# Optimization experiments

Hardware: AMD Instinct MI355X
Metric: run time of the kernel (lower is better)

The kernel has to match this reference:

```python
import jax, jax.numpy as jnp
import numpy as np

EPS = 1e-6  # eps assumed for rms/unit norm (repo uses a small eps; math identical up to eps)

def rms_norm(x):
    # normalize so RMS over last dim == 1
    return x * jax.lax.rsqrt(jnp.mean(x * x, axis=-1, keepdims=True) + EPS)

def unit_norm(w):
    # normalize each output row of the weight to unit L2 norm
    return w * jax.lax.rsqrt(jnp.sum(w * w, axis=-1, keepdims=True) + EPS)

def setup_inputs() -> dict:
    key = jax.random.key(0)
    k1, k2, k3 = jax.random.split(key, 3)
    B, S, D = 4, 2048, 2048
    x = jax.random.normal(k1, (B, S, D), dtype=jnp.float32)
    w_in = jax.random.normal(k2, (3 * D, D), dtype=jnp.float32)
    w_out = jax.random.normal(k3, (D, D), dtype=jnp.float32)
    return {"x": x, "w_in": w_in, "w_out": w_out}

def reference(x, w_in, w_out):
    B, S, D = x.shape
    H = 16
    hd = D // H
    # MPLinear in-projection with unit-normalized weight rows
    qkv = jnp.einsum("bsd,fd->bsf", x, unit_norm(w_in))  # [B,S,3D]
    qkv = qkv.reshape(B, S, 3, H, hd).transpose(2, 0, 3, 1, 4)  # [3,B,H,S,hd]
    q, k, v = qkv[0], qkv[1], qkv[2]
    q = rms_norm(q)
    k = rms_norm(k)
    # scaled dot product attention, causal, default scale 1/sqrt(hd)
    scores = jnp.einsum("bhqd,bhkd->bhqk", q, k) / jnp.sqrt(jnp.float32(hd))
    causal_mask = jnp.tril(jnp.ones((S, S), dtype=bool))
    scores = jnp.where(causal_mask, scores, jnp.finfo(scores.dtype).min)
    attn = jax.nn.softmax(scores, axis=-1)
    a = jnp.einsum("bhqk,bhkd->bhqd", attn, v)  # [B,H,S,hd]
    a = rms_norm(a)
    a = a.transpose(0, 2, 1, 3).reshape(B, S, D)
    return jnp.einsum("bsd,fd->bsf", a, unit_norm(w_out))
```

## Files before the change

### kernel.cpp

```cpp
#include <hip/hip_runtime.h>

typedef float f32x4 __attribute__((ext_vector_type(4)));
typedef __bf16 bf16x8 __attribute__((ext_vector_type(8)));

#define EPSF 1e-6f
#define AS1 __attribute__((address_space(1)))
#define AS3 __attribute__((address_space(3)))

__device__ static inline void gl_lds16(const __bf16* g, __bf16* l) {
  __builtin_amdgcn_global_load_lds((const AS1 void*)g, (AS3 void*)l, 16, 0, 0);
}

__global__ __launch_bounds__(256) void prep(const float* __restrict__ x,
                                            const float* __restrict__ w_in,
                                            const float* __restrict__ w_out,
                                            __bf16* __restrict__ xb,
                                            __bf16* __restrict__ w_in_n,
                                            __bf16* __restrict__ w_out_n) {
  __shared__ float red[4];
  const int bid = blockIdx.x;
  const int t = threadIdx.x;
  if (bid < 8192) {
    const float* src = (bid < 6144) ? (w_in + (size_t)bid * 2048)
                                    : (w_out + (size_t)(bid - 6144) * 2048);
    __bf16* dst = (bid < 6144) ? (w_in_n + (size_t)bid * 2048)
                               : (w_out_n + (size_t)(bid - 6144) * 2048);
    float4 v[2];
    float ss = 0.f;
#pragma unroll
    for (int i = 0; i < 2; i++) {
      v[i] = ((const float4*)src)[t + i * 256];
      ss += v[i].x * v[i].x + v[i].y * v[i].y + v[i].z * v[i].z + v[i].w * v[i].w;
    }
#pragma unroll
    for (int m = 32; m >= 1; m >>= 1) ss += __shfl_xor(ss, m);
    if ((t & 63) == 0) red[t >> 6] = ss;
    __syncthreads();
    float tot = red[0] + red[1] + red[2] + red[3];
    float sc = rsqrtf(tot + EPSF);
#pragma unroll
    for (int i = 0; i < 2; i++) {
      int c0 = (t + i * 256) * 4;
      dst[c0 + 0] = (__bf16)(v[i].x * sc);
      dst[c0 + 1] = (__bf16)(v[i].y * sc);
      dst[c0 + 2] = (__bf16)(v[i].z * sc);
      dst[c0 + 3] = (__bf16)(v[i].w * sc);
    }
  } else {
    size_t i = ((size_t)(bid - 8192) * 256 + t) * 8;
    float4 a = ((const float4*)(x + i))[0];
    float4 b = ((const float4*)(x + i))[1];
    bf16x8 o;
    o[0] = (__bf16)a.x; o[1] = (__bf16)a.y; o[2] = (__bf16)a.z; o[3] = (__bf16)a.w;
    o[4] = (__bf16)b.x; o[5] = (__bf16)b.y; o[6] = (__bf16)b.z; o[7] = (__bf16)b.w;
    *(bf16x8*)(xb + i) = o;
  }
}

#define LDSOFF(r_, blk_) ((r_) * 64 + (((blk_) ^ ((r_) & 7)) * 8))
#define SA(bb_, c_, kt_) gl_lds16(gA + (long)(c_) * 64 * K + (long)(kt_) * 64, &As[bb_][(c_) * 4096 + t * 8])
#define SB(bb_, c_, kt_) gl_lds16(gB + (long)(c_) * 64 * K + (long)(kt_) * 64, &Bs[bb_][(c_) * 4096 + t * 8])

template <int MODE>
__global__ __launch_bounds__(512) void gemm8(const __bf16* __restrict__ A,
                                             const __bf16* __restrict__ W,
                                             float* __restrict__ C,
                                             __bf16* __restrict__ Cb,
                                             __bf16* __restrict__ Vtb,
                                             int M, int N, int K) {
  __shared__ __bf16 As[2][16384];
  __shared__ __bf16 Bs[2][16384];
  __shared__ float rsum[8][128];

  const int gx = gridDim.x;
  const int nwg = gx * gridDim.y;
  int wg = blockIdx.y * gx + blockIdx.x;
  wg = (wg & 7) * (nwg >> 3) + (wg >> 3);
  const int bx = wg % gx, by = wg / gx;

  const int t = threadIdx.x;
  const int lane = t & 63, w = t >> 6;
  const int wr = w >> 2, wc = w & 3;
  const int wrb = wr * 128, wcb = wc * 64;
  const int fr = lane & 15, fq = lane >> 4;
  const long m0 = (long)by * 256;
  const long n0 = (long)bx * 256;
  const int NT = K >> 6;

  const int srow = t >> 3;
  const int sblk = (t & 7) ^ (srow & 7);
  const __bf16* gA = A + (m0 + srow) * (long)K + sblk * 8;
  const __bf16* gB = W + (n0 + srow) * (long)K + sblk * 8;

  f32x4 acc[8][4];
#pragma unroll
  for (int i = 0; i < 8; i++)
#pragma unroll
    for (int j = 0; j < 4; j++)
#pragma unroll
      for (int c = 0; c < 4; c++) acc[i][j][c] = 0.f;

  SA(0, 0, 0); SA(0, 1, 0); SA(0, 2, 0); SA(0, 3, 0);
  SB(0, 0, 0); SB(0, 1, 0); SB(0, 2, 0); SB(0, 3, 0);
  SA(1, 0, 1); SA(1, 2, 1);
  SB(1, 0, 1); SB(1, 1, 1); SB(1, 2, 1); SB(1, 3, 1);
  asm volatile("s_waitcnt vmcnt(6)" ::: "memory");
  __builtin_amdgcn_s_barrier();

  auto tile_step = [&](int kt, int b) {
    bf16x8 a0[4][2], b01[2][2];
#pragma unroll
    for (int i = 0; i < 4; i++)
#pragma unroll
      for (int ks = 0; ks < 2; ks++)
        a0[i][ks] = *(const bf16x8*)&As[b][LDSOFF(wrb + i * 16 + fr, ks * 4 + fq)];
#pragma unroll
    for (int j = 0; j < 2; j++)
#pragma unroll
      for (int ks = 0; ks < 2; ks++)
        b01[j][ks] = *(const bf16x8*)&Bs[b][LDSOFF(wcb + j * 16 + fr, ks * 4 + fq)];
    if (kt + 1 < NT) { SA(b ^ 1, 1, kt + 1); SA(b ^ 1, 3, kt + 1); }
    __builtin_amdgcn_s_setprio(1);
#pragma unroll
    for (int i = 0; i < 4; i++)
#pragma unroll
      for (int j = 0; j < 2; j++)
#pragma unroll
        for (int ks = 0; ks < 2; ks++)
          acc[i][j] = __builtin_amdgcn_mfma_f32_16x16x32_bf16(a0[i][ks], b01[j][ks], acc[i][j], 0, 0, 0);
    __builtin_amdgcn_s_setprio(0);
    __builtin_amdgcn_sched_barrier(0);
    __builtin_amdgcn_s_barrier();

    bf16x8 b23[2][2];
#pragma unroll
    for (int j = 0; j < 2; j++)
#pragma unroll
      for (int ks = 0; ks < 2; ks++)
        b23[j][ks] = *(const bf16x8*)&Bs[b][LDSOFF(wcb + (2 + j) * 16 + fr, ks * 4 + fq)];
    if (kt + 2 < NT) { SA(b, 0, kt + 2); SA(b, 2, kt + 2); }
    __builtin_amdgcn_s_setprio(1);
#pragma unroll
    for (int i = 0; i < 4; i++)
#pragma unroll
      for (int j = 0; j < 2; j++)
#pragma unroll
        for (int ks = 0; ks < 2; ks++)
          acc[i][2 + j] = __builtin_amdgcn_mfma_f32_16x16x32_bf16(a0[i][ks], b23[j][ks], acc[i][2 + j], 0, 0, 0);
    __builtin_amdgcn_s_setprio(0);
    __builtin_amdgcn_sched_barrier(0);
    __builtin_amdgcn_s_barrier();

    bf16x8 a1[4][2];
#pragma unroll
    for (int i = 0; i < 4; i++)
#pragma unroll
      for (int ks = 0; ks < 2; ks++)
        a1[i][ks] = *(const bf16x8*)&As[b][LDSOFF(wrb + 64 + i * 16 + fr, ks * 4 + fq)];
    if (kt + 2 < NT) { SB(b, 0, kt + 2); SB(b, 1, kt + 2); SB(b, 2, kt + 2); SB(b, 3, kt + 2); }
    __builtin_amdgcn_s_setprio(1);
#pragma unroll
    for (int i = 0; i < 4; i++)
#pragma unroll
      for (int j = 0; j < 2; j++)
#pragma unroll
        for (int ks = 0; ks < 2; ks++)
          acc[4 + i][j] = __builtin_amdgcn_mfma_f32_16x16x32_bf16(a1[i][ks], b01[j][ks], acc[4 + i][j], 0, 0, 0);
#pragma unroll
    for (int i = 0; i < 4; i++)
#pragma unroll
      for (int j = 0; j < 2; j++)
#pragma unroll
        for (int ks = 0; ks < 2; ks++)
          acc[4 + i][2 + j] = __builtin_amdgcn_mfma_f32_16x16x32_bf16(a1[i][ks], b23[j][ks], acc[4 + i][2 + j], 0, 0, 0);
    __builtin_amdgcn_s_setprio(0);
    if (kt >= NT - 2)
      asm volatile("s_waitcnt vmcnt(0)" ::: "memory");
    else
      asm volatile("s_waitcnt vmcnt(6)" ::: "memory");
    __builtin_amdgcn_sched_barrier(0);
    __builtin_amdgcn_s_barrier();
  };

  for (int kt = 0; kt < NT; kt += 2) {
    tile_step(kt, 0);
    tile_step(kt + 1, 1);
  }

  if (MODE == 0) {
#pragma unroll
    for (int i = 0; i < 8; i++)
#pragma unroll
      for (int j = 0; j < 4; j++)
#pragma unroll
        for (int r = 0; r < 4; r++) {
          long row = m0 + wrb + i * 16 + fq * 4 + r;
          long col = n0 + wcb + j * 16 + fr;
          C[row * N + col] = acc[i][j][r];
        }
  } else {
    const int tt = (int)(n0 >> 11);
    const int hh = (int)(((n0 >> 7) + (wc >> 1)) & 15);
    const long e0 = (long)(wc & 1) * 64;
    if (tt < 2) {
#pragma unroll
      for (int i = 0; i < 8; i++)
#pragma unroll
        for (int r = 0; r < 4; r++) {
          float s2 = 0.f;
#pragma unroll
          for (int j = 0; j < 4; j++) s2 += acc[i][j][r] * acc[i][j][r];
          s2 += __shfl_xor(s2, 1);
          s2 += __shfl_xor(s2, 2);
          s2 += __shfl_xor(s2, 4);
          s2 += __shfl_xor(s2, 8);
          if (fr == 0) rsum[w][i * 16 + fq * 4 + r] = s2;
        }
      __syncthreads();
#pragma unroll
      for (int i = 0; i < 8; i++)
#pragma unroll
        for (int r = 0; r < 4; r++) {
          int rl = i * 16 + fq * 4 + r;
          float tot = rsum[w][rl] + rsum[w ^ 1][rl];
          float sc = rsqrtf(tot * (1.f / 128.f) + EPSF);
          long row = m0 + wrb + rl;
          long bb = row >> 11, ss = row & 2047;
          __bf16* base = Cb + ((((long)tt * 4 + bb) * 16 + hh) * 2048 + ss) * 128 + e0;
#pragma unroll
          for (int j = 0; j < 4; j++)
            base[j * 16 + fr] = (__bf16)(acc[i][j][r] * sc);
        }
    } else {
#pragma unroll
      for (int i = 0; i < 8; i++)
#pragma unroll
        for (int r = 0; r < 4; r++) {
          long row = m0 + wrb + i * 16 + fq * 4 + r;
          long bb = row >> 11, ss = row & 2047;
#pragma unroll
          for (int j = 0; j < 4; j++)
            Vtb[((bb * 16 + hh) * 128 + e0 + j * 16 + fr) * 2048 + ss] = (__bf16)acc[i][j][r];
        }
    }
  }
}

__global__ __launch_bounds__(512) void attn(const __bf16* __restrict__ qkv,
                                            const __bf16* __restrict__ vt,
                                            __bf16* __restrict__ an) {
  __shared__ __bf16 Ks[64 * 128];
  __shared__ __bf16 Vs[128 * 64];
  __shared__ __bf16 plds[8][16 * 40];
  const int L = blockIdx.x;
  const int qt = L >> 6;
  const int bh = (L & 7) + 8 * ((L >> 3) & 7);
  const int t = threadIdx.x;
  const int lane = t & 63, w = t >> 6;
  const int fr = lane & 15, fq = lane >> 4;
  const int swz = fr & 7;
  const __bf16* Q = qkv + (long)bh * 262144;
  const __bf16* Kbh = qkv + 16777216L + (long)bh * 262144;
  const __bf16* Vbh = vt + (long)bh * 262144;
  __bf16* pw = plds[w];
  const float sc2 = 0.08838834764831845f * 1.4426950408889634f;
  const float MFIX = 20.0f;
  const int b = bh >> 4, h = bh & 15;

  const __bf16* gK = Kbh + (long)(t >> 4) * 128 + ((t & 15) ^ ((t >> 4) & 7)) * 8;
  const __bf16* gV = Vbh + (long)(t >> 3) * 2048 + ((t & 7) ^ ((t >> 3) & 7)) * 8;
  __bf16* lK = &Ks[t * 8];
  __bf16* lV = &Vs[t * 8];

#pragma unroll 1
  for (int side = 0; side < 2; side++) {
    const int qi = side ? (15 - qt) : qt;
    const int q0 = qi * 128 + w * 16;
    const int cha = q0 >> 5;
    bf16x8 qf[4];
#pragma unroll
    for (int ec = 0; ec < 4; ec++)
      qf[ec] = *(const bf16x8*)(Q + (long)(q0 + fr) * 128 + ec * 32 + fq * 8);
    float lacc[4];
#pragma unroll
    for (int r = 0; r < 4; r++) lacc[r] = 0.f;
    f32x4 oacc[8];
#pragma unroll
    for (int e = 0; e < 8; e++)
#pragma unroll
      for (int c = 0; c < 4; c++) oacc[e][c] = 0.f;

    const int nst = 2 * qi + 2;
#pragma unroll 1
    for (int st = 0; st < nst; st++) {
      const int k0 = st * 64;
      gl_lds16(gK + (long)k0 * 128, lK);
      gl_lds16(gK + (long)(k0 + 32) * 128, lK + 4096);
      gl_lds16(gV + k0, lV);
      gl_lds16(gV + 64L * 2048 + k0, lV + 4096);
      __syncthreads();
#pragma unroll
      for (int half = 0; half < 2; half++) {
        const int k32 = k0 + half * 32;
        const int ch = k32 >> 5;
        if (ch <= cha) {
          f32x4 sa[2];
#pragma unroll
          for (int ct = 0; ct < 2; ct++)
#pragma unroll
            for (int c = 0; c < 4; c++) sa[ct][c] = 0.f;
#pragma unroll
          for (int ct = 0; ct < 2; ct++) {
#pragma unroll
            for (int ec = 0; ec < 4; ec++) {
              bf16x8 kf = *(const bf16x8*)(&Ks[(half * 32 + ct * 16 + fr) * 128 +
                                               ((ec * 4 + fq) ^ swz) * 8]);
              sa[ct] = __builtin_amdgcn_mfma_f32_16x16x32_bf16(qf[ec], kf, sa[ct], 0, 0, 0);
            }
          }
          if (ch == cha) {
#pragma unroll
            for (int r = 0; r < 4; r++) {
              int qg = q0 + fq * 4 + r;
              float p0 = exp2f(((k32 + fr) <= qg) ? sa[0][r] * sc2 - MFIX : -1e30f);
              float p1 = exp2f(((k32 + 16 + fr) <= qg) ? sa[1][r] * sc2 - MFIX : -1e30f);
              lacc[r] += p0 + p1;
              pw[(fq * 4 + r) * 40 + fr] = (__bf16)p0;
              pw[(fq * 4 + r) * 40 + 16 + fr] = (__bf16)p1;
            }
          } else {
#pragma unroll
            for (int r = 0; r < 4; r++) {
              float p0 = exp2f(__builtin_fmaf(sa[0][r], sc2, -MFIX));
              float p1 = exp2f(__builtin_fmaf(sa[1][r], sc2, -MFIX));
              lacc[r] += p0 + p1;
              pw[(fq * 4 + r) * 40 + fr] = (__bf16)p0;
              pw[(fq * 4 + r) * 40 + 16 + fr] = (__bf16)p1;
            }
          }
          bf16x8 pa = *(const bf16x8*)(&pw[fr * 40 + fq * 8]);
#pragma unroll
          for (int e = 0; e < 8; e++) {
            bf16x8 vf = *(const bf16x8*)(&Vs[(e * 16 + fr) * 64 +
                                             ((half * 4 + fq) ^ swz) * 8]);
            oacc[e] = __builtin_amdgcn_mfma_f32_16x16x32_bf16(pa, vf, oacc[e], 0, 0, 0);
          }
        }
      }
      __syncthreads();
    }
#pragma unroll
    for (int r = 0; r < 4; r++) {
      float ls = lacc[r];
      ls += __shfl_xor(ls, 1);
      ls += __shfl_xor(ls, 2);
      ls += __shfl_xor(ls, 4);
      ls += __shfl_xor(ls, 8);
      float inv = 1.0f / ls;
      float ssq = 0.f;
#pragma unroll
      for (int e = 0; e < 8; e++) { float v = oacc[e][r] * inv; ssq += v * v; }
      ssq += __shfl_xor(ssq, 1);
      ssq += __shfl_xor(ssq, 2);
      ssq += __shfl_xor(ssq, 4);
      ssq += __shfl_xor(ssq, 8);
      float rsc = rsqrtf(ssq * (1.f / 128.f) + EPSF) * inv;
      long s = q0 + fq * 4 + r;
      __bf16* dst = an + ((long)b * 2048 + s) * 2048 + h * 128;
#pragma unroll
      for (int e = 0; e < 8; e++) dst[e * 16 + fr] = (__bf16)(oacc[e][r] * rsc);
    }
  }
}

extern "C" void kernel_launch(void* const* d_in, const int* in_sizes, int n_in,
                              void* d_out, int out_size, void* d_ws, size_t ws_size,
                              hipStream_t stream) {
  const float* x = (const float*)d_in[0];
  const float* w_in = (const float*)d_in[1];
  const float* w_out = (const float*)d_in[2];
  float* out = (float*)d_out;
  char* ws = (char*)d_ws;

  __bf16* w_in_n = (__bf16*)(ws);
  __bf16* w_out_n = (__bf16*)(ws + 25165824);
  __bf16* xb = (__bf16*)(ws + 33554432);
  __bf16* an = xb;
  __bf16* qkv = (__bf16*)(ws + 67108864);
  __bf16* vt = (__bf16*)(ws + 167772160);

  prep<<<16384, 256, 0, stream>>>(x, w_in, w_out, xb, w_in_n, w_out_n);
  gemm8<1><<<dim3(24, 32), 512, 0, stream>>>(xb, w_in_n, nullptr, qkv, vt, 8192, 6144, 2048);
  attn<<<512, 512, 0, stream>>>(qkv, vt, an);
  gemm8<0><<<dim3(8, 32), 512, 0, stream>>>(an, w_out_n, out, nullptr, nullptr, 8192, 2048, 2048);
}
```

Before: 513.9 us.

## Double-buffer K/V tiles in attention with async global-to-LDS prefetch

The attention kernel now keeps two LDS buffers for K and V and issues the next-but-one tile's global_load_lds before computing the current tile. Manual vmcnt waits and raw barriers replace the full __syncthreads, so memory latency can overlap with the MFMA work. This doubles K/V LDS use, which may reduce occupancy. Correctness depends on the vmcnt counting: the Q fragment loads are issued after the prefetch, so the counts must stay consistent.

```diff
diff --git a/kernel.cpp b/kernel.cpp
--- a/kernel.cpp
+++ b/kernel.cpp
@@ -249,8 +249,8 @@
 __global__ __launch_bounds__(512) void attn(const __bf16* __restrict__ qkv,
                                             const __bf16* __restrict__ vt,
                                             __bf16* __restrict__ an) {
-  __shared__ __bf16 Ks[64 * 128];
-  __shared__ __bf16 Vs[128 * 64];
+  __shared__ __bf16 Ks[2][64 * 128];
+  __shared__ __bf16 Vs[2][128 * 64];
   __shared__ __bf16 plds[8][16 * 40];
   const int L = blockIdx.x;
   const int qt = L >> 6;
@@ -269,14 +269,24 @@
 
   const __bf16* gK = Kbh + (long)(t >> 4) * 128 + ((t & 15) ^ ((t >> 4) & 7)) * 8;
   const __bf16* gV = Vbh + (long)(t >> 3) * 2048 + ((t & 7) ^ ((t >> 3) & 7)) * 8;
-  __bf16* lK = &Ks[t * 8];
-  __bf16* lV = &Vs[t * 8];
+
+  auto stage = [&](int st, int buf) {
+    const long k0 = (long)st * 64;
+    gl_lds16(gK + k0 * 128, &Ks[buf][t * 8]);
+    gl_lds16(gK + (k0 + 32) * 128, &Ks[buf][4096 + t * 8]);
+    gl_lds16(gV + k0, &Vs[buf][t * 8]);
+    gl_lds16(gV + 64L * 2048 + k0, &Vs[buf][4096 + t * 8]);
+  };
 
 #pragma unroll 1
   for (int side = 0; side < 2; side++) {
     const int qi = side ? (15 - qt) : qt;
     const int q0 = qi * 128 + w * 16;
     const int cha = q0 >> 5;
+    const int nst = 2 * qi + 2;
+
+    stage(0, 0);
+    stage(1, 1);
     bf16x8 qf[4];
 #pragma unroll
     for (int ec = 0; ec < 4; ec++)
@@ -290,15 +300,16 @@
 #pragma unroll
       for (int c = 0; c < 4; c++) oacc[e][c] = 0.f;
 
-    const int nst = 2 * qi + 2;
 #pragma unroll 1
     for (int st = 0; st < nst; st++) {
+      if (st + 1 < nst)
+        asm volatile("s_waitcnt vmcnt(4)" ::: "memory");
+      else
+        asm volatile("s_waitcnt vmcnt(0)" ::: "memory");
+      __builtin_amdgcn_s_barrier();
+      const __bf16* Kb = Ks[st & 1];
+      const __bf16* Vb = Vs[st & 1];
       const int k0 = st * 64;
-      gl_lds16(gK + (long)k0 * 128, lK);
-      gl_lds16(gK + (long)(k0 + 32) * 128, lK + 4096);
-      gl_lds16(gV + k0, lV);
-      gl_lds16(gV + 64L * 2048 + k0, lV + 4096);
-      __syncthreads();
 #pragma unroll
       for (int half = 0; half < 2; half++) {
         const int k32 = k0 + half * 32;
@@ -313,7 +324,7 @@
           for (int ct = 0; ct < 2; ct++) {
 #pragma unroll
             for (int ec = 0; ec < 4; ec++) {
-              bf16x8 kf = *(const bf16x8*)(&Ks[(half * 32 + ct * 16 + fr) * 128 +
+              bf16x8 kf = *(const bf16x8*)(&Kb[(half * 32 + ct * 16 + fr) * 128 +
                                                ((ec * 4 + fq) ^ swz) * 8]);
               sa[ct] = __builtin_amdgcn_mfma_f32_16x16x32_bf16(qf[ec], kf, sa[ct], 0, 0, 0);
             }
@@ -341,13 +352,14 @@
           bf16x8 pa = *(const bf16x8*)(&pw[fr * 40 + fq * 8]);
 #pragma unroll
           for (int e = 0; e < 8; e++) {
-            bf16x8 vf = *(const bf16x8*)(&Vs[(e * 16 + fr) * 64 +
+            bf16x8 vf = *(const bf16x8*)(&Vb[(e * 16 + fr) * 64 +
                                              ((half * 4 + fq) ^ swz) * 8]);
             oacc[e] = __builtin_amdgcn_mfma_f32_16x16x32_bf16(pa, vf, oacc[e], 0, 0, 0);
           }
         }
       }
-      __syncthreads();
+      __builtin_amdgcn_s_barrier();
+      if (st + 2 < nst) stage(st + 2, st & 1);
     }
 #pragma unroll
     for (int r = 0; r < 4; r++) {
```

Result: slower. 531.4 us (+3.4%).

## Give each attention wave two query fragments and halve block threads

Applied to the files above, without the earlier changes.

The attention kernel now runs 256 threads per block, and each wave handles 32 query rows as two 16-row fragments instead of one. Every K and V fragment read from LDS is reused for two MFMAs, which halves LDS read traffic per MFMA and raises MFMA density. The K/V tile loads are split into four 16-byte global-to-LDS copies per thread. The cost is roughly double the accumulator and Q registers per thread (the launch bound requests 3 blocks per CU) and fewer waves per block to hide latency.

```diff
diff --git a/kernel.cpp b/kernel.cpp
--- a/kernel.cpp
+++ b/kernel.cpp
@@ -246,9 +246,9 @@
   }
 }
 
-__global__ __launch_bounds__(512) void attn(const __bf16* __restrict__ qkv,
-                                            const __bf16* __restrict__ vt,
-                                            __bf16* __restrict__ an) {
+__global__ __launch_bounds__(256, 3) void attn(const __bf16* __restrict__ qkv,
+                                               const __bf16* __restrict__ vt,
+                                               __bf16* __restrict__ an) {
   __shared__ __bf16 Ks[64 * 128];
   __shared__ __bf16 Vs[128 * 64];
   __shared__ __bf16 plds[8][16 * 40];
@@ -262,7 +262,6 @@
   const __bf16* Q = qkv + (long)bh * 262144;
   const __bf16* Kbh = qkv + 16777216L + (long)bh * 262144;
   const __bf16* Vbh = vt + (long)bh * 262144;
-  __bf16* pw = plds[w];
   const float sc2 = 0.08838834764831845f * 1.4426950408889634f;
   const float MFIX = 20.0f;
   const int b = bh >> 4, h = bh & 15;
@@ -275,101 +274,118 @@
 #pragma unroll 1
   for (int side = 0; side < 2; side++) {
     const int qi = side ? (15 - qt) : qt;
-    const int q0 = qi * 128 + w * 16;
+    const int q0 = qi * 128 + w * 32;
     const int cha = q0 >> 5;
-    bf16x8 qf[4];
-#pragma unroll
-    for (int ec = 0; ec < 4; ec++)
-      qf[ec] = *(const bf16x8*)(Q + (long)(q0 + fr) * 128 + ec * 32 + fq * 8);
-    float lacc[4];
-#pragma unroll
-    for (int r = 0; r < 4; r++) lacc[r] = 0.f;
-    f32x4 oacc[8];
-#pragma unroll
-    for (int e = 0; e < 8; e++)
-#pragma unroll
-      for (int c = 0; c < 4; c++) oacc[e][c] = 0.f;
+    bf16x8 qf[2][4];
+#pragma unroll
+    for (int f = 0; f < 2; f++)
+#pragma unroll
+      for (int ec = 0; ec < 4; ec++)
+        qf[f][ec] = *(const bf16x8*)(Q + (long)(q0 + f * 16 + fr) * 128 + ec * 32 + fq * 8);
+    float lacc[2][4];
+#pragma unroll
+    for (int f = 0; f < 2; f++)
+#pragma unroll
+      for (int r = 0; r < 4; r++) lacc[f][r] = 0.f;
+    f32x4 oacc[2][8];
+#pragma unroll
+    for (int f = 0; f < 2; f++)
+#pragma unroll
+      for (int e = 0; e < 8; e++)
+#pragma unroll
+        for (int c = 0; c < 4; c++) oacc[f][e][c] = 0.f;
 
     const int nst = 2 * qi + 2;
 #pragma unroll 1
     for (int st = 0; st < nst; st++) {
-      const int k0 = st * 64;
-      gl_lds16(gK + (long)k0 * 128, lK);
-      gl_lds16(gK + (long)(k0 + 32) * 128, lK + 4096);
-      gl_lds16(gV + k0, lV);
-      gl_lds16(gV + 64L * 2048 + k0, lV + 4096);
+      const long k0 = (long)st * 64;
+#pragma unroll
+      for (int j = 0; j < 4; j++) gl_lds16(gK + (k0 + j * 16) * 128, lK + j * 2048);
+#pragma unroll
+      for (int j = 0; j < 4; j++) gl_lds16(gV + (long)j * 32 * 2048 + k0, lV + j * 2048);
       __syncthreads();
 #pragma unroll
       for (int half = 0; half < 2; half++) {
-        const int k32 = k0 + half * 32;
+        const int k32 = (int)k0 + half * 32;
         const int ch = k32 >> 5;
         if (ch <= cha) {
-          f32x4 sa[2];
-#pragma unroll
-          for (int ct = 0; ct < 2; ct++)
-#pragma unroll
-            for (int c = 0; c < 4; c++) sa[ct][c] = 0.f;
+          f32x4 sa[2][2];
+#pragma unroll
+          for (int f = 0; f < 2; f++)
+#pragma unroll
+            for (int ct = 0; ct < 2; ct++)
+#pragma unroll
+              for (int c = 0; c < 4; c++) sa[f][ct][c] = 0.f;
 #pragma unroll
           for (int ct = 0; ct < 2; ct++) {
 #pragma unroll
             for (int ec = 0; ec < 4; ec++) {
               bf16x8 kf = *(const bf16x8*)(&Ks[(half * 32 + ct * 16 + fr) * 128 +
                                                ((ec * 4 + fq) ^ swz) * 8]);
-              sa[ct] = __builtin_amdgcn_mfma_f32_16x16x32_bf16(qf[ec], kf, sa[ct], 0, 0, 0);
+              sa[0][ct] = __builtin_amdgcn_mfma_f32_16x16x32_bf16(qf[0][ec], kf, sa[0][ct], 0, 0, 0);
+              sa[1][ct] = __builtin_amdgcn_mfma_f32_16x16x32_bf16(qf[1][ec], kf, sa[1][ct], 0, 0, 0);
             }
           }
-          if (ch == cha) {
-#pragma unroll
-            for (int r = 0; r < 4; r++) {
-              int qg = q0 + fq * 4 + r;
-              float p0 = exp2f(((k32 + fr) <= qg) ? sa[0][r] * sc2 - MFIX : -1e30f);
-              float p1 = exp2f(((k32 + 16 + fr) <= qg) ? sa[1][r] * sc2 - MFIX : -1e30f);
-              lacc[r] += p0 + p1;
-              pw[(fq * 4 + r) * 40 + fr] = (__bf16)p0;
-              pw[(fq * 4 + r) * 40 + 16 + fr] = (__bf16)p1;
-            }
-          } else {
-#pragma unroll
-            for (int r = 0; r < 4; r++) {
-              float p0 = exp2f(__builtin_fmaf(sa[0][r], sc2, -MFIX));
-              float p1 = exp2f(__builtin_fmaf(sa[1][r], sc2, -MFIX));
-              lacc[r] += p0 + p1;
-              pw[(fq * 4 + r) * 40 + fr] = (__bf16)p0;
-              pw[(fq * 4 + r) * 40 + 16 + fr] = (__bf16)p1;
+#pragma unroll
+          for (int f = 0; f < 2; f++) {
+            __bf16* pwf = plds[(w << 1) + f];
+            if (ch == cha) {
+#pragma unroll
+              for (int r = 0; r < 4; r++) {
+                int qg = q0 + f * 16 + fq * 4 + r;
+                float p0 = exp2f(((k32 + fr) <= qg) ? sa[f][0][r] * sc2 - MFIX : -1e30f);
+                float p1 = exp2f(((k32 + 16 + fr) <= qg) ? sa[f][1][r] * sc2 - MFIX : -1e30f);
+                lacc[f][r] += p0 + p1;
+                pwf[(fq * 4 + r) * 40 + fr] = (__bf16)p0;
+                pwf[(fq * 4 + r) * 40 + 16 + fr] = (__bf16)p1;
+              }
+            } else {
+#pragma unroll
+              for (int r = 0; r < 4; r++) {
+                float p0 = exp2f(__builtin_fmaf(sa[f][0][r], sc2, -MFIX));
+                float p1 = exp2f(__builtin_fmaf(sa[f][1][r], sc2, -MFIX));
+                lacc[f][r] += p0 + p1;
+                pwf[(fq * 4 + r) * 40 + fr] = (__bf16)p0;
+                pwf[(fq * 4 + r) * 40 + 16 + fr] = (__bf16)p1;
+              }
             }
           }
-          bf16x8 pa = *(const bf16x8*)(&pw[fr * 40 + fq * 8]);
+          bf16x8 pa0 = *(const bf16x8*)(&plds[(w << 1) + 0][fr * 40 + fq * 8]);
+          bf16x8 pa1 = *(const bf16x8*)(&plds[(w << 1) + 1][fr * 40 + fq * 8]);
 #pragma unroll
           for (int e = 0; e < 8; e++) {
             bf16x8 vf = *(const bf16x8*)(&Vs[(e * 16 + fr) * 64 +
                                              ((half * 4 + fq) ^ swz) * 8]);
-            oacc[e] = __builtin_amdgcn_mfma_f32_16x16x32_bf16(pa, vf, oacc[e], 0, 0, 0);
+            oacc[0][e] = __builtin_amdgcn_mfma_f32_16x16x32_bf16(pa0, vf, oacc[0][e], 0, 0, 0);
+            oacc[1][e] = __builtin_amdgcn_mfma_f32_16x16x32_bf16(pa1, vf, oacc[1][e], 0, 0, 0);
           }
         }
       }
       __syncthreads();
     }
 #pragma unroll
-    for (int r = 0; r < 4; r++) {
-      float ls = lacc[r];
-      ls += __shfl_xor(ls, 1);
-      ls += __shfl_xor(ls, 2);
-      ls += __shfl_xor(ls, 4);
-      ls += __shfl_xor(ls, 8);
-      float inv = 1.0f / ls;
-      float ssq = 0.f;
-#pragma unroll
-      for (int e = 0; e < 8; e++) { float v = oacc[e][r] * inv; ssq += v * v; }
-      ssq += __shfl_xor(ssq, 1);
-      ssq += __shfl_xor(ssq, 2);
-      ssq += __shfl_xor(ssq, 4);
-      ssq += __shfl_xor(ssq, 8);
-      float rsc = rsqrtf(ssq * (1.f / 128.f) + EPSF) * inv;
-      long s = q0 + fq * 4 + r;
-      __bf16* dst = an + ((long)b * 2048 + s) * 2048 + h * 128;
-#pragma unroll
-      for (int e = 0; e < 8; e++) dst[e * 16 + fr] = (__bf16)(oacc[e][r] * rsc);
-    }
+    for (int f = 0; f < 2; f++)
+#pragma unroll
+      for (int r = 0; r < 4; r++) {
+        float ls = lacc[f][r];
+        ls += __shfl_xor(ls, 1);
+        ls += __shfl_xor(ls, 2);
+        ls += __shfl_xor(ls, 4);
+        ls += __shfl_xor(ls, 8);
+        float inv = 1.0f / ls;
+        float ssq = 0.f;
+#pragma unroll
+        for (int e = 0; e < 8; e++) { float v = oacc[f][e][r] * inv; ssq += v * v; }
+        ssq += __shfl_xor(ssq, 1);
+        ssq += __shfl_xor(ssq, 2);
+        ssq += __shfl_xor(ssq, 4);
+        ssq += __shfl_xor(ssq, 8);
+        float rsc = rsqrtf(ssq * (1.f / 128.f) + EPSF) * inv;
+        long s = q0 + f * 16 + fq * 4 + r;
+        __bf16* dst = an + ((long)b * 2048 + s) * 2048 + h * 128;
+#pragma unroll
+        for (int e = 0; e < 8; e++) dst[e * 16 + fr] = (__bf16)(oacc[f][e][r] * rsc);
+      }
   }
 }
 
@@ -391,6 +407,6 @@
 
   prep<<<16384, 256, 0, stream>>>(x, w_in, w_out, xb, w_in_n, w_out_n);
   gemm8<1><<<dim3(24, 32), 512, 0, stream>>>(xb, w_in_n, nullptr, qkv, vt, 8192, 6144, 2048);
-  attn<<<512, 512, 0, stream>>>(qkv, vt, an);
+  attn<<<512, 256, 0, stream>>>(qkv, vt, an);
   gemm8<0><<<dim3(8, 32), 512, 0, stream>>>(an, w_out_n, out, nullptr, nullptr, 8192, 2048, 2048);
 }
```

Result: no change. 517.9 us (+0.8%).
